# Optimization experiments

Hardware: AMD Instinct MI355X
Metric: run time of the kernel (lower is better)

## Reference

```python
import jax, jax.numpy as jnp
import numpy as np

B, K, T, C = 4, 8, 2048, 64

def setup_inputs() -> dict:
    key = jax.random.key(0)
    ks = jax.random.split(key, 7)
    return {
        "x": jax.random.normal(ks[0], (B, K, T, C), dtype=jnp.float32),
        "Wq": jax.random.normal(ks[1], (C, C), dtype=jnp.float32) / np.sqrt(C),
        "bq": jax.random.normal(ks[2], (C,), dtype=jnp.float32) * 0.01,
        "Wk": jax.random.normal(ks[3], (C, C), dtype=jnp.float32) / np.sqrt(C),
        "bk": jax.random.normal(ks[4], (C,), dtype=jnp.float32) * 0.01,
        "Wv": jax.random.normal(ks[5], (C, C), dtype=jnp.float32) / np.sqrt(C),
        "bv": jax.random.normal(ks[6], (C,), dtype=jnp.float32) * 0.01,
    }

def reference(x, Wq, bq, Wk, bk, Wv, bv):
    c_dim = x.shape[-1]
    # torch nn.Linear: y = x @ W.T + b
    q = jnp.einsum('bktc,dc->bktd', x, Wq) + bq
    k = jnp.einsum('bktc,dc->bktd', x, Wk) + bk
    v = jnp.einsum('bktc,dc->bktd', x, Wv) + bv
    scores = jnp.einsum('bkic,bkjc->bkij', q, k) / jnp.sqrt(jnp.float32(c_dim))
    attn = jax.nn.softmax(scores, axis=-1)
    out = jnp.einsum('bkij,bkjc->bkic', attn, v)
    return out
```

## Files before the change

### kernel.cpp

```cpp
#include <hip/hip_runtime.h>


#define T_DIM 2048
#define NHEAD 32
#define HSTRIDE (T_DIM * 64)
#define QSCALE 0.18033688011112042f
#define SOFF  8.0f

#define SWZ(row, grp) ((row) * 64 + ((((grp) ^ ((row) & 7)) & 7) * 8))

#define RAW_BARRIER() asm volatile("s_waitcnt lgkmcnt(0)\n\ts_barrier" ::: "memory")

typedef _Float16 h8 __attribute__((ext_vector_type(8)));
typedef _Float16 h4 __attribute__((ext_vector_type(4)));
typedef __fp16   g2 __attribute__((ext_vector_type(2)));
typedef float    f4 __attribute__((ext_vector_type(4)));
typedef float    fv16 __attribute__((ext_vector_type(16)));

union H4U { h4 v; g2 p[2]; };
union H8U { h8 v; h4 h[2]; g2 p[4]; };

#if defined(__has_builtin)
#if __has_builtin(__builtin_amdgcn_exp2f)
#define EXP2(x) __builtin_amdgcn_exp2f(x)
#endif
#endif
#ifndef EXP2
__device__ inline float exp2_raw(float x) {
    float r;
    asm("v_exp_f32 %0, %1" : "=v"(r) : "v"(x));
    return r;
}
#define EXP2(x) exp2_raw(x)
#endif

__device__ inline h4 cvt4(f4 x) {
    H4U u;
    u.p[0] = __builtin_amdgcn_cvt_pkrtz(x[0], x[1]);
    u.p[1] = __builtin_amdgcn_cvt_pkrtz(x[2], x[3]);
    return u.v;
}

__device__ inline h8 cvt8(f4 a, f4 b) {
    H8U r;
    r.h[0] = cvt4(a);
    r.h[1] = cvt4(b);
    return r.v;
}

__device__ inline fv16 splat16(float x) {
    fv16 r;
    #pragma unroll
    for (int i = 0; i < 16; ++i) r[i] = x;
    return r;
}

__global__ __launch_bounds__(256) void qkv_proj_kernel(
    const float* __restrict__ x,
    const float* __restrict__ Wq, const float* __restrict__ bq,
    const float* __restrict__ Wk, const float* __restrict__ bk,
    const float* __restrict__ Wv, const float* __restrict__ bv,
    _Float16* __restrict__ qh, _Float16* __restrict__ khT,
    _Float16* __restrict__ vtT)
{
    __shared__ _Float16 ws[3][64 * 64];
    __shared__ float bsh[3][64];

    const int tid  = threadIdx.x;
    const int row0 = blockIdx.x * 64;
    const int head = blockIdx.x >> 5;
    const int t0   = (blockIdx.x & 31) * 64;

    const int w    = tid >> 6;
    const int lane = tid & 63;
    const int l15  = lane & 15;
    const int qd   = lane >> 4;

    f4 xa[2][2];
    {
        const float* xp = x + (size_t)(row0 + w * 16 + l15) * 64 + qd * 8;
        #pragma unroll
        for (int ch = 0; ch < 2; ++ch) {
            xa[ch][0] = *(const f4*)(xp + ch * 32);
            xa[ch][1] = *(const f4*)(xp + ch * 32 + 4);
        }
    }

    #pragma unroll
    for (int m = 0; m < 3; ++m) {
        const float* Wm = (m == 0) ? Wq : ((m == 1) ? Wk : Wv);
        const float* bm = (m == 0) ? bq : ((m == 1) ? bk : bv);
        #pragma unroll
        for (int pass = 0; pass < 4; ++pass) {
            const int idx = pass * 1024 + tid * 4;
            const int d = idx >> 6, c = idx & 63;
            f4 wv = *(const f4*)(Wm + idx);
            *(h4*)&ws[m][SWZ(d, c >> 3) + (c & 7)] = cvt4(wv);
        }
        if (tid < 64) bsh[m][tid] = bm[tid];
    }

    h8 af[2];
    #pragma unroll
    for (int ch = 0; ch < 2; ++ch)
        af[ch] = cvt8(xa[ch][0], xa[ch][1]);

    __syncthreads();

    f4 acc[3][4];
    #pragma unroll
    for (int m = 0; m < 3; ++m) {
        h8 bf[4][2];
        #pragma unroll
        for (int ns = 0; ns < 4; ++ns)
            #pragma unroll
            for (int ch = 0; ch < 2; ++ch)
                bf[ns][ch] = *(const h8*)&ws[m][SWZ(ns * 16 + l15, ch * 4 + qd)];
        #pragma unroll
        for (int ns = 0; ns < 4; ++ns)
            acc[m][ns] = (f4){0.f, 0.f, 0.f, 0.f};
        #pragma unroll
        for (int ch = 0; ch < 2; ++ch)
            #pragma unroll
            for (int ns = 0; ns < 4; ++ns)
                acc[m][ns] = __builtin_amdgcn_mfma_f32_16x16x32_f16(
                    af[ch], bf[ns][ch], acc[m][ns], 0, 0, 0);
    }

    __syncthreads();

    #pragma unroll
    for (int m = 0; m < 2; ++m) {
        #pragma unroll
        for (int ns = 0; ns < 4; ++ns) {
            const int d = ns * 16 + l15;
            const float bias = bsh[m][d];
            #pragma unroll
            for (int r = 0; r < 4; ++r) {
                const int t = w * 16 + qd * 4 + r;
                float v = acc[m][ns][r] + bias;
                if (m == 0) v *= QSCALE;
                ws[m][SWZ(t, d >> 3) + (d & 7)] = (_Float16)v;
            }
        }
    }
    #pragma unroll
    for (int ns = 0; ns < 4; ++ns) {
        const int d = ns * 16 + l15;
        const float bias = bsh[2][d];
        const int tl = w * 16 + qd * 4;
        f4 pvf;
        #pragma unroll
        for (int r = 0; r < 4; ++r)
            pvf[r] = acc[2][ns][r] + bias;
        *(h4*)&ws[2][SWZ(d, tl >> 3) + (tl & 7)] = cvt4(pvf);
    }

    __syncthreads();

    #pragma unroll
    for (int pass = 0; pass < 2; ++pass) {
        const int t  = pass * 32 + (tid >> 3);
        const int c0 = (tid & 7) * 8;
        *(h8*)&qh[(size_t)(row0 + t) * 64 + c0] =
            *(const h8*)&ws[0][SWZ(t, tid & 7)];
    }
    #pragma unroll
    for (int pass = 0; pass < 2; ++pass) {
        const int f   = pass * 2048 + tid * 8;
        const int kb  = f >> 11;
        const int cs  = (f >> 9) & 3;
        const int l   = (f >> 3) & 63;
        const int p   = l & 31;
        const int w16 = p & 15;
        const int sw  = ((w16 & 12) == 4) ? (w16 + 4)
                      : (((w16 & 12) == 8) ? (w16 - 4) : w16);
        const int tact = kb * 32 + (p & 16) + sw;
        const int g8   = cs * 2 + (l >> 5);
        *(h8*)&khT[(size_t)head * HSTRIDE + (t0 >> 6) * 4096 + f] =
            *(const h8*)&ws[1][SWZ(tact, g8)];
    }
    #pragma unroll
    for (int pass = 0; pass < 2; ++pass) {
        const int f  = pass * 2048 + tid * 8;
        const int q2 = f >> 9;
        const int b  = q2 >> 1, cc = q2 & 1;
        const int l  = (f >> 3) & 63;
        const int c  = cc * 32 + (l & 31);
        const int tg = b * 2 + (l >> 5);
        *(h8*)&vtT[(size_t)head * HSTRIDE + (t0 >> 6) * 4096 + f] =
            *(const h8*)&ws[2][SWZ(c, tg)];
    }
}

__global__ __launch_bounds__(384, 2) void attn_kernel(
    const _Float16* __restrict__ qh, const _Float16* __restrict__ khT,
    const _Float16* __restrict__ vtT, float* __restrict__ out)
{
    __shared__ _Float16 tiles[3][8192];
    const int tid  = threadIdx.x;
    const int w    = tid >> 6;
    const int lane = tid & 63;

    const int bid  = blockIdx.x;
    const int xcd  = bid & 7;
    const int slot = bid >> 3;
    const int head = xcd * 4 + (slot >> 3);
    const int qpart = slot & 7;

    if (w < 4) {
        const int q0  = qpart * 256 + w * 64;
        const int l31 = lane & 31;
        const int lh  = lane >> 5;

        h8 qf[2][4];
        #pragma unroll
        for (int qs = 0; qs < 2; ++qs) {
            const _Float16* qp = qh + (size_t)(head * T_DIM + q0 + qs * 32 + l31) * 64 + lh * 8;
            #pragma unroll
            for (int cs = 0; cs < 4; ++cs)
                qf[qs][cs] = *(const h8*)(qp + cs * 16);
        }

        f4 rs4[2] = {(f4){0.f,0.f,0.f,0.f}, (f4){0.f,0.f,0.f,0.f}};
        fv16 oacc[2][2];
        #pragma unroll
        for (int qs = 0; qs < 2; ++qs)
            #pragma unroll
            for (int cc = 0; cc < 2; ++cc)
                oacc[qs][cc] = splat16(0.f);

        const int ko = lane * 8;
        const _Float16* c0 = &tiles[0][0];
        const _Float16* c1 = &tiles[1][0];
        const _Float16* c2 = &tiles[2][0];

        __syncthreads();

        fv16 st[2][2];
        #pragma unroll
        for (int kb = 0; kb < 2; ++kb) {
            h8 kf[4];
            #pragma unroll
            for (int cs = 0; cs < 4; ++cs)
                kf[cs] = *(const h8*)(c0 + kb * 2048 + cs * 512 + ko);
            st[kb][0] = splat16(-SOFF);
            st[kb][1] = splat16(-SOFF);
            #pragma unroll
            for (int cs = 0; cs < 4; ++cs)
                #pragma unroll
                for (int qs = 0; qs < 2; ++qs)
                    st[kb][qs] = __builtin_amdgcn_mfma_f32_32x32x16_f16(
                        kf[cs], qf[qs][cs], st[kb][qs], 0, 0, 0);
        }

        for (int it = 0; it < 32; ++it) {
            const bool more = (it < 31);

            h8 kf[2][4];
            if (more) {
                #pragma unroll
                for (int kb = 0; kb < 2; ++kb)
                    #pragma unroll
                    for (int cs = 0; cs < 4; ++cs)
                        kf[kb][cs] = *(const h8*)(c1 + kb * 2048 + cs * 512 + ko);
            }
            h8 vf[4][2];
            #pragma unroll
            for (int b = 0; b < 4; ++b)
                #pragma unroll
                for (int cc = 0; cc < 2; ++cc)
                    vf[b][cc] = *(const h8*)(c0 + 4096 + (b * 2 + cc) * 512 + ko);

            #pragma unroll
            for (int kb = 0; kb < 2; ++kb)
                #pragma unroll
                for (int qs = 0; qs < 2; ++qs) {
                    f4 p[2];
                    #pragma unroll
                    for (int g = 0; g < 4; ++g) {
                        p[g >> 1][(g & 1) * 2 + 0] = 0.f;
                    }
                    f4 pg[4];
                    #pragma unroll
                    for (int g = 0; g < 4; ++g) {
                        pg[g][0] = EXP2(st[kb][qs][4 * g + 0]);
                        pg[g][1] = EXP2(st[kb][qs][4 * g + 1]);
                        pg[g][2] = EXP2(st[kb][qs][4 * g + 2]);
                        pg[g][3] = EXP2(st[kb][qs][4 * g + 3]);
                        rs4[qs] += pg[g];
                    }

                    if (more) {
                        st[kb][qs] = splat16(-SOFF);
                        #pragma unroll
                        for (int cs = 0; cs < 4; ++cs)
                            st[kb][qs] = __builtin_amdgcn_mfma_f32_32x32x16_f16(
                                kf[kb][cs], qf[qs][cs], st[kb][qs], 0, 0, 0);
                    }

                    H8U pa[2];
                    #pragma unroll
                    for (int g = 0; g < 4; ++g) {
                        pa[g >> 1].p[(g & 1) * 2 + 0] = __builtin_amdgcn_cvt_pkrtz(pg[g][0], pg[g][1]);
                        pa[g >> 1].p[(g & 1) * 2 + 1] = __builtin_amdgcn_cvt_pkrtz(pg[g][2], pg[g][3]);
                    }
                    #pragma unroll
                    for (int bl = 0; bl < 2; ++bl) {
                        const int b = kb * 2 + bl;
                        #pragma unroll
                        for (int cc = 0; cc < 2; ++cc)
                            oacc[qs][cc] = __builtin_amdgcn_mfma_f32_32x32x16_f16(
                                pa[bl].v, vf[b][cc], oacc[qs][cc], 0, 0, 0);
                    }
                }

            const _Float16* tmp = c0; c0 = c1; c1 = c2; c2 = tmp;
            __syncthreads();
        }

        #pragma unroll
        for (int qs = 0; qs < 2; ++qs) {
            float lsum = (rs4[qs][0] + rs4[qs][1]) + (rs4[qs][2] + rs4[qs][3]);
            lsum += __shfl_xor(lsum, 32, 64);
            const float linv = 1.f / lsum;
            #pragma unroll
            for (int r = 0; r < 16; ++r) {
                const int qrow = (r & 3) + 8 * (r >> 2) + 4 * lh;
                const float fac = __shfl(linv, qrow, 64);
                #pragma unroll
                for (int cc = 0; cc < 2; ++cc)
                    out[(size_t)(head * T_DIM + q0 + qs * 32 + qrow) * 64 + cc * 32 + l31] =
                        oacc[qs][cc][r] * fac;
            }
        }
    } else {
        const _Float16* src = ((w == 4) ? khT : vtT) + (size_t)head * HSTRIDE;
        const int off = (w - 4) * 4096;
        _Float16* d0 = &tiles[0][off];
        _Float16* d1 = &tiles[1][off];
        _Float16* d2 = &tiles[2][off];
        const int lo = lane * 8;
        h8 sA[8], sB[8];

        #pragma unroll
        for (int b = 0; b < 8; ++b) sA[b] = *(const h8*)(src + b * 512 + lo);
        #pragma unroll
        for (int b = 0; b < 8; ++b) sB[b] = *(const h8*)(src + 4096 + b * 512 + lo);
        #pragma unroll
        for (int b = 0; b < 8; ++b) *(h8*)(d0 + b * 512 + lo) = sA[b];
        #pragma unroll
        for (int b = 0; b < 8; ++b) *(h8*)(d1 + b * 512 + lo) = sB[b];
        #pragma unroll
        for (int b = 0; b < 8; ++b) sA[b] = *(const h8*)(src + 8192 + b * 512 + lo);
        const _Float16* sp = src + 3 * 4096;
        RAW_BARRIER();

        _Float16* w0 = d2;
        _Float16* w1 = d0;
        _Float16* w2 = d1;

        for (int t2 = 0; t2 < 16; ++t2) {
            if (t2 < 15) {
                #pragma unroll
                for (int b = 0; b < 8; ++b) sB[b] = *(const h8*)(sp + b * 512 + lo);
                sp += 4096;
                #pragma unroll
                for (int b = 0; b < 8; ++b) *(h8*)(w0 + b * 512 + lo) = sA[b];
            }
            RAW_BARRIER();
            { _Float16* t = w0; w0 = w1; w1 = w2; w2 = t; }
            if (t2 < 14) {
                #pragma unroll
                for (int b = 0; b < 8; ++b) sA[b] = *(const h8*)(sp + b * 512 + lo);
                sp += 4096;
            }
            if (t2 < 15) {
                #pragma unroll
                for (int b = 0; b < 8; ++b) *(h8*)(w0 + b * 512 + lo) = sB[b];
            }
            RAW_BARRIER();
            { _Float16* t = w0; w0 = w1; w1 = w2; w2 = t; }
        }
    }
}

extern "C" void kernel_launch(void* const* d_in, const int* in_sizes, int n_in,
                              void* d_out, int out_size, void* d_ws, size_t ws_size,
                              hipStream_t stream)
{
    (void)in_sizes; (void)n_in; (void)out_size; (void)ws_size;
    const float* x  = (const float*)d_in[0];
    const float* Wq = (const float*)d_in[1];
    const float* bq = (const float*)d_in[2];
    const float* Wk = (const float*)d_in[3];
    const float* bk = (const float*)d_in[4];
    const float* Wv = (const float*)d_in[5];
    const float* bv = (const float*)d_in[6];
    float* out = (float*)d_out;

    _Float16* qh  = (_Float16*)d_ws;
    _Float16* khT = qh + (size_t)NHEAD * HSTRIDE;
    _Float16* vtT = khT + (size_t)NHEAD * HSTRIDE;

    hipLaunchKernelGGL(qkv_proj_kernel, dim3(1024), dim3(256), 0, stream,
                       x, Wq, bq, Wk, bk, Wv, bv, qh, khT, vtT);
    hipLaunchKernelGGL(attn_kernel, dim3(256), dim3(384), 0, stream,
                       qh, khT, vtT, out);
}
```

Measured before the change: 135.4 us.

## Split key range across wave pairs, load K/V directly into registers

Replaces the producer/consumer LDS triple-buffered attention kernel with one in which each pair of waves splits the key sequence in half and reads K/V fragments straight from global memory into registers, prefetching the next tile. The partial output accumulators and row sums are exchanged through shared memory at the end and combined before normalization. The grid doubles to 512 blocks of 256 threads. This removes the per-iteration barriers and LDS staging, at the cost of redundant global/L2 reads of K/V by every wave and the extra final reduction.

```diff
diff --git a/kernel.cpp b/kernel.cpp
--- a/kernel.cpp
+++ b/kernel.cpp
@@ -8,8 +8,6 @@
 #define SOFF  8.0f
 
 #define SWZ(row, grp) ((row) * 64 + ((((grp) ^ ((row) & 7)) & 7) * 8))
-
-#define RAW_BARRIER() asm volatile("s_waitcnt lgkmcnt(0)\n\ts_barrier" ::: "memory")
 
 typedef _Float16 h8 __attribute__((ext_vector_type(8)));
 typedef _Float16 h4 __attribute__((ext_vector_type(4)));
@@ -193,195 +191,159 @@
     }
 }
 
-__global__ __launch_bounds__(384, 2) void attn_kernel(
+__global__ __launch_bounds__(256, 2) void attn_kernel(
     const _Float16* __restrict__ qh, const _Float16* __restrict__ khT,
     const _Float16* __restrict__ vtT, float* __restrict__ out)
 {
-    __shared__ _Float16 tiles[3][8192];
+    __shared__ float xbuf[4][2304];
+
     const int tid  = threadIdx.x;
     const int w    = tid >> 6;
     const int lane = tid & 63;
+    const int l31  = lane & 31;
+    const int lh   = lane >> 5;
+    const int qg   = w >> 1;
+    const int ph   = w & 1;
 
     const int bid  = blockIdx.x;
     const int xcd  = bid & 7;
     const int slot = bid >> 3;
-    const int head = xcd * 4 + (slot >> 3);
-    const int qpart = slot & 7;
-
-    if (w < 4) {
-        const int q0  = qpart * 256 + w * 64;
-        const int l31 = lane & 31;
-        const int lh  = lane >> 5;
-
-        h8 qf[2][4];
-        #pragma unroll
-        for (int qs = 0; qs < 2; ++qs) {
-            const _Float16* qp = qh + (size_t)(head * T_DIM + q0 + qs * 32 + l31) * 64 + lh * 8;
+    const int head = xcd * 4 + (slot >> 4);
+    const int qpart = slot & 15;
+    const int q0   = qpart * 128 + qg * 64;
+
+    h8 qf[2][4];
+    #pragma unroll
+    for (int qs = 0; qs < 2; ++qs) {
+        const _Float16* qp = qh + (size_t)(head * T_DIM + q0 + qs * 32 + l31) * 64 + lh * 8;
+        #pragma unroll
+        for (int cs = 0; cs < 4; ++cs)
+            qf[qs][cs] = *(const h8*)(qp + cs * 16);
+    }
+
+    const int ko = lane * 8;
+    const _Float16* kbase = khT + (size_t)head * HSTRIDE + (size_t)ph * 16 * 4096;
+    const _Float16* vbase = vtT + (size_t)head * HSTRIDE + (size_t)ph * 16 * 4096;
+
+    f4 rs4[2] = {(f4){0.f,0.f,0.f,0.f}, (f4){0.f,0.f,0.f,0.f}};
+    fv16 oacc[2][2];
+    #pragma unroll
+    for (int qs = 0; qs < 2; ++qs)
+        #pragma unroll
+        for (int cc = 0; cc < 2; ++cc)
+            oacc[qs][cc] = splat16(0.f);
+
+    h8 kf[2][4];
+    h8 vf[4][2];
+    #pragma unroll
+    for (int kb = 0; kb < 2; ++kb)
+        #pragma unroll
+        for (int cs = 0; cs < 4; ++cs)
+            kf[kb][cs] = *(const h8*)(kbase + kb * 2048 + cs * 512 + ko);
+    #pragma unroll
+    for (int b = 0; b < 4; ++b)
+        #pragma unroll
+        for (int cc = 0; cc < 2; ++cc)
+            vf[b][cc] = *(const h8*)(vbase + (b * 2 + cc) * 512 + ko);
+
+    for (int it = 0; it < 16; ++it) {
+        const _Float16* kn = kbase + (size_t)(it + 1) * 4096;
+        const _Float16* vn = vbase + (size_t)(it + 1) * 4096;
+        const bool more = (it < 15);
+
+        #pragma unroll
+        for (int kb = 0; kb < 2; ++kb) {
+            fv16 st2[2];
+            st2[0] = splat16(-SOFF);
+            st2[1] = splat16(-SOFF);
             #pragma unroll
             for (int cs = 0; cs < 4; ++cs)
-                qf[qs][cs] = *(const h8*)(qp + cs * 16);
-        }
-
-        f4 rs4[2] = {(f4){0.f,0.f,0.f,0.f}, (f4){0.f,0.f,0.f,0.f}};
-        fv16 oacc[2][2];
-        #pragma unroll
-        for (int qs = 0; qs < 2; ++qs)
-            #pragma unroll
-            for (int cc = 0; cc < 2; ++cc)
-                oacc[qs][cc] = splat16(0.f);
-
-        const int ko = lane * 8;
-        const _Float16* c0 = &tiles[0][0];
-        const _Float16* c1 = &tiles[1][0];
-        const _Float16* c2 = &tiles[2][0];
-
-        __syncthreads();
-
-        fv16 st[2][2];
-        #pragma unroll
-        for (int kb = 0; kb < 2; ++kb) {
-            h8 kf[4];
-            #pragma unroll
-            for (int cs = 0; cs < 4; ++cs)
-                kf[cs] = *(const h8*)(c0 + kb * 2048 + cs * 512 + ko);
-            st[kb][0] = splat16(-SOFF);
-            st[kb][1] = splat16(-SOFF);
-            #pragma unroll
-            for (int cs = 0; cs < 4; ++cs)
                 #pragma unroll
                 for (int qs = 0; qs < 2; ++qs)
-                    st[kb][qs] = __builtin_amdgcn_mfma_f32_32x32x16_f16(
-                        kf[cs], qf[qs][cs], st[kb][qs], 0, 0, 0);
-        }
-
-        for (int it = 0; it < 32; ++it) {
-            const bool more = (it < 31);
-
-            h8 kf[2][4];
+                    st2[qs] = __builtin_amdgcn_mfma_f32_32x32x16_f16(
+                        kf[kb][cs], qf[qs][cs], st2[qs], 0, 0, 0);
+
             if (more) {
                 #pragma unroll
-                for (int kb = 0; kb < 2; ++kb)
+                for (int cs = 0; cs < 4; ++cs)
+                    kf[kb][cs] = *(const h8*)(kn + kb * 2048 + cs * 512 + ko);
+            }
+
+            #pragma unroll
+            for (int qs = 0; qs < 2; ++qs) {
+                f4 pg[4];
+                #pragma unroll
+                for (int g = 0; g < 4; ++g) {
+                    pg[g][0] = EXP2(st2[qs][4 * g + 0]);
+                    pg[g][1] = EXP2(st2[qs][4 * g + 1]);
+                    pg[g][2] = EXP2(st2[qs][4 * g + 2]);
+                    pg[g][3] = EXP2(st2[qs][4 * g + 3]);
+                    rs4[qs] += pg[g];
+                }
+                H8U pa[2];
+                #pragma unroll
+                for (int g = 0; g < 4; ++g) {
+                    pa[g >> 1].p[(g & 1) * 2 + 0] = __builtin_amdgcn_cvt_pkrtz(pg[g][0], pg[g][1]);
+                    pa[g >> 1].p[(g & 1) * 2 + 1] = __builtin_amdgcn_cvt_pkrtz(pg[g][2], pg[g][3]);
+                }
+                #pragma unroll
+                for (int bl = 0; bl < 2; ++bl)
                     #pragma unroll
-                    for (int cs = 0; cs < 4; ++cs)
-                        kf[kb][cs] = *(const h8*)(c1 + kb * 2048 + cs * 512 + ko);
+                    for (int cc = 0; cc < 2; ++cc)
+                        oacc[qs][cc] = __builtin_amdgcn_mfma_f32_32x32x16_f16(
+                            pa[bl].v, vf[kb * 2 + bl][cc], oacc[qs][cc], 0, 0, 0);
             }
-            h8 vf[4][2];
-            #pragma unroll
-            for (int b = 0; b < 4; ++b)
-                #pragma unroll
-                for (int cc = 0; cc < 2; ++cc)
-                    vf[b][cc] = *(const h8*)(c0 + 4096 + (b * 2 + cc) * 512 + ko);
-
-            #pragma unroll
-            for (int kb = 0; kb < 2; ++kb)
-                #pragma unroll
-                for (int qs = 0; qs < 2; ++qs) {
-                    f4 p[2];
+
+            if (more) {
+                #pragma unroll
+                for (int bl = 0; bl < 2; ++bl)
                     #pragma unroll
-                    for (int g = 0; g < 4; ++g) {
-                        p[g >> 1][(g & 1) * 2 + 0] = 0.f;
-                    }
-                    f4 pg[4];
-                    #pragma unroll
-                    for (int g = 0; g < 4; ++g) {
-                        pg[g][0] = EXP2(st[kb][qs][4 * g + 0]);
-                        pg[g][1] = EXP2(st[kb][qs][4 * g + 1]);
-                        pg[g][2] = EXP2(st[kb][qs][4 * g + 2]);
-                        pg[g][3] = EXP2(st[kb][qs][4 * g + 3]);
-                        rs4[qs] += pg[g];
-                    }
-
-                    if (more) {
-                        st[kb][qs] = splat16(-SOFF);
-                        #pragma unroll
-                        for (int cs = 0; cs < 4; ++cs)
-                            st[kb][qs] = __builtin_amdgcn_mfma_f32_32x32x16_f16(
-                                kf[kb][cs], qf[qs][cs], st[kb][qs], 0, 0, 0);
-                    }
-
-                    H8U pa[2];
-                    #pragma unroll
-                    for (int g = 0; g < 4; ++g) {
-                        pa[g >> 1].p[(g & 1) * 2 + 0] = __builtin_amdgcn_cvt_pkrtz(pg[g][0], pg[g][1]);
-                        pa[g >> 1].p[(g & 1) * 2 + 1] = __builtin_amdgcn_cvt_pkrtz(pg[g][2], pg[g][3]);
-                    }
-                    #pragma unroll
-                    for (int bl = 0; bl < 2; ++bl) {
-                        const int b = kb * 2 + bl;
-                        #pragma unroll
-                        for (int cc = 0; cc < 2; ++cc)
-                            oacc[qs][cc] = __builtin_amdgcn_mfma_f32_32x32x16_f16(
-                                pa[bl].v, vf[b][cc], oacc[qs][cc], 0, 0, 0);
-                    }
-                }
-
-            const _Float16* tmp = c0; c0 = c1; c1 = c2; c2 = tmp;
-            __syncthreads();
-        }
-
-        #pragma unroll
-        for (int qs = 0; qs < 2; ++qs) {
-            float lsum = (rs4[qs][0] + rs4[qs][1]) + (rs4[qs][2] + rs4[qs][3]);
-            lsum += __shfl_xor(lsum, 32, 64);
-            const float linv = 1.f / lsum;
-            #pragma unroll
-            for (int r = 0; r < 16; ++r) {
-                const int qrow = (r & 3) + 8 * (r >> 2) + 4 * lh;
-                const float fac = __shfl(linv, qrow, 64);
-                #pragma unroll
-                for (int cc = 0; cc < 2; ++cc)
-                    out[(size_t)(head * T_DIM + q0 + qs * 32 + qrow) * 64 + cc * 32 + l31] =
-                        oacc[qs][cc][r] * fac;
+                    for (int cc = 0; cc < 2; ++cc)
+                        vf[kb * 2 + bl][cc] =
+                            *(const h8*)(vn + ((kb * 2 + bl) * 2 + cc) * 512 + ko);
             }
         }
-    } else {
-        const _Float16* src = ((w == 4) ? khT : vtT) + (size_t)head * HSTRIDE;
-        const int off = (w - 4) * 4096;
-        _Float16* d0 = &tiles[0][off];
-        _Float16* d1 = &tiles[1][off];
-        _Float16* d2 = &tiles[2][off];
-        const int lo = lane * 8;
-        h8 sA[8], sB[8];
-
-        #pragma unroll
-        for (int b = 0; b < 8; ++b) sA[b] = *(const h8*)(src + b * 512 + lo);
-        #pragma unroll
-        for (int b = 0; b < 8; ++b) sB[b] = *(const h8*)(src + 4096 + b * 512 + lo);
-        #pragma unroll
-        for (int b = 0; b < 8; ++b) *(h8*)(d0 + b * 512 + lo) = sA[b];
-        #pragma unroll
-        for (int b = 0; b < 8; ++b) *(h8*)(d1 + b * 512 + lo) = sB[b];
-        #pragma unroll
-        for (int b = 0; b < 8; ++b) sA[b] = *(const h8*)(src + 8192 + b * 512 + lo);
-        const _Float16* sp = src + 3 * 4096;
-        RAW_BARRIER();
-
-        _Float16* w0 = d2;
-        _Float16* w1 = d0;
-        _Float16* w2 = d1;
-
-        for (int t2 = 0; t2 < 16; ++t2) {
-            if (t2 < 15) {
-                #pragma unroll
-                for (int b = 0; b < 8; ++b) sB[b] = *(const h8*)(sp + b * 512 + lo);
-                sp += 4096;
-                #pragma unroll
-                for (int b = 0; b < 8; ++b) *(h8*)(w0 + b * 512 + lo) = sA[b];
-            }
-            RAW_BARRIER();
-            { _Float16* t = w0; w0 = w1; w1 = w2; w2 = t; }
-            if (t2 < 14) {
-                #pragma unroll
-                for (int b = 0; b < 8; ++b) sA[b] = *(const h8*)(sp + b * 512 + lo);
-                sp += 4096;
-            }
-            if (t2 < 15) {
-                #pragma unroll
-                for (int b = 0; b < 8; ++b) *(h8*)(w0 + b * 512 + lo) = sB[b];
-            }
-            RAW_BARRIER();
-            { _Float16* t = w0; w0 = w1; w1 = w2; w2 = t; }
-        }
+    }
+
+    const int wqs = ph ^ 1;
+    {
+        float* xb = xbuf[w];
+        #pragma unroll
+        for (int cc = 0; cc < 2; ++cc)
+            #pragma unroll
+            for (int r = 0; r < 16; ++r)
+                xb[(cc * 16 + r) * 64 + lane] = oacc[wqs][cc][r];
+        #pragma unroll
+        for (int i = 0; i < 4; ++i)
+            xb[2048 + i * 64 + lane] = rs4[wqs][i];
+    }
+
+    __syncthreads();
+
+    const float* pb = xbuf[w ^ 1];
+    const int f = ph;
+    fv16 of[2];
+    #pragma unroll
+    for (int cc = 0; cc < 2; ++cc)
+        #pragma unroll
+        for (int r = 0; r < 16; ++r)
+            of[cc][r] = oacc[f][cc][r] + pb[(cc * 16 + r) * 64 + lane];
+    f4 rsf;
+    #pragma unroll
+    for (int i = 0; i < 4; ++i)
+        rsf[i] = rs4[f][i] + pb[2048 + i * 64 + lane];
+
+    float lsum = (rsf[0] + rsf[1]) + (rsf[2] + rsf[3]);
+    lsum += __shfl_xor(lsum, 32, 64);
+    const float linv = 1.f / lsum;
+    #pragma unroll
+    for (int r = 0; r < 16; ++r) {
+        const int qrow = (r & 3) + 8 * (r >> 2) + 4 * lh;
+        const float fac = __shfl(linv, qrow, 64);
+        #pragma unroll
+        for (int cc = 0; cc < 2; ++cc)
+            out[(size_t)(head * T_DIM + q0 + f * 32 + qrow) * 64 + cc * 32 + l31] =
+                of[cc][r] * fac;
     }
 }
 
@@ -405,6 +367,6 @@
 
     hipLaunchKernelGGL(qkv_proj_kernel, dim3(1024), dim3(256), 0, stream,
                        x, Wq, bq, Wk, bk, Wv, bv, qh, khT, vtT);
-    hipLaunchKernelGGL(attn_kernel, dim3(256), dim3(384), 0, stream,
+    hipLaunchKernelGGL(attn_kernel, dim3(512), dim3(256), 0, stream,
                        qh, khT, vtT, out);
 }
```

Result: no change. 134.1 us (-1.0%).
